# Performance work log

Measured on AMD Instinct MI355X. Metric: run time of the kernel, lower is better.

## Reference

```python
import jax, jax.numpy as jnp
import numpy as np

N = 100_000      # points
DEG = 16         # uniform neighbor count
E = N * DEG      # edges
NB = 4           # radial basis count (n)
MB = 4           # angular basis count (m)
FIN = 8
FOUT = 8
SUPPORT = 2.0    # module-level `support` constant in the original source


def _rbf_linear(nb, x, periodic):
    # evalRBFSeries(..., which='linear', epsilon=1.0): hat functions on [-1,1]
    if periodic:
        spacing = 2.0 / nb
        centroids = jnp.linspace(-1.0, 1.0, nb + 1)[:nb]          # [nb]
        ra = x[None, :] - centroids[:, None]                       # [nb, E]
        d = jnp.minimum(jnp.minimum(jnp.abs(ra), jnp.abs(ra - 2.0)), jnp.abs(ra + 2.0)) / spacing
    else:
        spacing = 2.0 / (nb - 1)
        centroids = jnp.linspace(-1.0, 1.0, nb)
        d = jnp.abs(x[None, :] - centroids[:, None]) / spacing     # [nb, E]
    return jnp.clip(1.0 - d, 0.0, 1.0)


def setup_inputs() -> dict:
    key = jax.random.key(0)
    k1, k2, k3, k4 = jax.random.split(key, 4)
    positions = jax.random.uniform(k1, (N, 2), dtype=jnp.float32)
    features = jax.random.normal(k2, (N, FIN), dtype=jnp.float32)
    # neighbors: DEG per point, never self (avoids zero-distance edges)
    offs = jax.random.randint(k3, (E,), 1, N)
    base = jnp.repeat(jnp.arange(N, dtype=jnp.int32), DEG)
    neighbors = ((base + offs) % N).astype(jnp.int32)
    row_splits = (jnp.arange(N + 1, dtype=jnp.int32) * DEG)
    # glorot_normal for kernel [fout, fin, n, m]
    kernel = jax.random.normal(k4, (FOUT, FIN, NB, MB), dtype=jnp.float32) * np.float32(
        np.sqrt(2.0 / ((FIN + FOUT) * NB * MB)))
    return {"positions": positions, "features": features, "kernel": kernel,
            "neighbors": neighbors, "row_splits": row_splits}


def reference(positions, features, kernel, neighbors, row_splits):
    n_pts = positions.shape[0]
    n_edges = neighbors.shape[0]
    counts = row_splits[1:] - row_splits[:-1]                       # [N]
    seg = jnp.repeat(jnp.arange(n_pts, dtype=jnp.int32), counts,
                     total_repeat_length=n_edges)                   # [E] owning point per edge
    rel = positions[neighbors] - positions[seg]                     # [E, 2]
    r = jnp.linalg.norm(rel, axis=1) / SUPPORT                      # [E]
    theta = jnp.arctan2(rel[:, 1], rel[:, 0])                       # [E]
    c = _rbf_linear(NB, r * 2.0 - 1.0, periodic=False)              # [NB, E]
    f = _rbf_linear(MB, theta / np.float32(np.pi), periodic=True)   # [MB, E]
    M = jnp.einsum('un,vn->nuv', c, f)                              # [E, NB, MB] per-edge outer product
    O = jnp.einsum('unm,ijnm->uij', M, kernel)                      # [E, FOUT, FIN]
    fv = features[neighbors]                                        # [E, FIN]
    FO = jnp.einsum('nij,nj->ni', O, fv)                            # [E, FOUT]
    return jax.ops.segment_sum(FO, seg, num_segments=n_pts)         # [N, FOUT]
```

## Files before the change

kernel.cpp:

```cpp
#include <hip/hip_runtime.h>
#include <math.h>


#define FIN 8
#define FOUT 8

__global__ __launch_bounds__(256) void rbf_kernel(
    const float* __restrict__ positions,
    const float* __restrict__ features,
    const float* __restrict__ kern,
    const int*   __restrict__ neighbors,
    const int*   __restrict__ row_splits,
    float*       __restrict__ out,
    int npts)
{
    __shared__ float Kl[1024];
    {
        const float4* src = (const float4*)kern;
        float4* dst = (float4*)Kl;
        if (threadIdx.x < 256) dst[threadIdx.x] = src[threadIdx.x];
    }
    __syncthreads();

    int gt   = blockIdx.x * blockDim.x + threadIdx.x;
    int u    = gt >> 1;
    int half = gt & 1;
    if (u >= npts) return;

    float2 pu = ((const float2*)positions)[u];
    int rs0 = row_splits[u];
    int rs1 = row_splits[u + 1];

    float g[16][4];
#pragma unroll
    for (int nm = 0; nm < 16; ++nm)
#pragma unroll
        for (int j = 0; j < 4; ++j) g[nm][j] = 0.0f;

    const float INV_PI = 0.31830988618379067f;

    for (int e = rs0; e < rs1; ++e) {
        int nb = neighbors[e];
        float2 pn = ((const float2*)positions)[nb];
        float dx = pn.x - pu.x;
        float dy = pn.y - pu.y;
        float dist = sqrtf(dx * dx + dy * dy);
        float tr = dist * 1.5f;
        float theta = atan2f(dy, dx);
        float ta = fmaf(theta, INV_PI, 1.0f) * 2.0f;

        float c[4], f[4];
#pragma unroll
        for (int n = 0; n < 4; ++n) {
            float d = fabsf(tr - (float)n);
            c[n] = fmaxf(1.0f - d, 0.0f);
        }
#pragma unroll
        for (int m = 0; m < 4; ++m) {
            float d0 = fabsf(ta - (float)m);
            float d1 = fabsf(ta - (float)m - 4.0f);
            float d2 = fabsf(ta - (float)m + 4.0f);
            float d  = fminf(d0, fminf(d1, d2));
            f[m] = fmaxf(1.0f - d, 0.0f);
        }

        float4 fv = ((const float4*)features)[nb * 2 + half];
        float fvj[4] = {fv.x, fv.y, fv.z, fv.w};

#pragma unroll
        for (int n = 0; n < 4; ++n)
#pragma unroll
            for (int m = 0; m < 4; ++m) {
                float w = c[n] * f[m];
#pragma unroll
                for (int j = 0; j < 4; ++j)
                    g[n * 4 + m][j] = fmaf(w, fvj[j], g[n * 4 + m][j]);
            }
    }

    float o[8];
#pragma unroll
    for (int i = 0; i < 8; ++i) o[i] = 0.0f;

    const float4* K4 = (const float4*)Kl;
#pragma unroll
    for (int i = 0; i < 8; ++i) {
#pragma unroll
        for (int j = 0; j < 4; ++j) {
            int jg = half * 4 + j;
            int base4 = (i * 128 + jg * 16) >> 2;
#pragma unroll
            for (int q = 0; q < 4; ++q) {
                float4 kv = K4[base4 + q];
                o[i] = fmaf(kv.x, g[q * 4 + 0][j], o[i]);
                o[i] = fmaf(kv.y, g[q * 4 + 1][j], o[i]);
                o[i] = fmaf(kv.z, g[q * 4 + 2][j], o[i]);
                o[i] = fmaf(kv.w, g[q * 4 + 3][j], o[i]);
            }
        }
    }

#pragma unroll
    for (int i = 0; i < 8; ++i)
        o[i] += __shfl_xor(o[i], 1);

    float4 ov = (half == 0) ? make_float4(o[0], o[1], o[2], o[3])
                            : make_float4(o[4], o[5], o[6], o[7]);
    ((float4*)out)[u * 2 + half] = ov;
}

extern "C" void kernel_launch(void* const* d_in, const int* in_sizes, int n_in,
                              void* d_out, int out_size, void* d_ws, size_t ws_size,
                              hipStream_t stream) {
    const float* positions  = (const float*)d_in[0];
    const float* features   = (const float*)d_in[1];
    const float* kern       = (const float*)d_in[2];
    const int*   neighbors  = (const int*)d_in[3];
    const int*   row_splits = (const int*)d_in[4];
    float* out = (float*)d_out;

    int npts = in_sizes[0] / 2;
    int total = npts * 2;
    int block = 256;
    int grid = (total + block - 1) / block;
    rbf_kernel<<<grid, block, 0, stream>>>(positions, features, kern,
                                           neighbors, row_splits, out, npts);
}
```

Before: 106.7 us.

## Split each point's edges across four lanes and batch neighbor gathers

Each point is now handled by four threads instead of two: two feature halves times two edge halves. Partial sums are combined with an extra xor-shuffle before the write. For the common 16-neighbor case, neighbor indices are read as int4 vectors and the position and feature gathers are issued four at a time, so more loads are in flight per thread. This doubles thread count and adds more latency hiding, at the cost of duplicated geometry and atan2 work across the feature halves and an extra shuffle stage.

```diff
diff --git a/kernel.cpp b/kernel.cpp
--- a/kernel.cpp
+++ b/kernel.cpp
@@ -23,13 +23,16 @@
     __syncthreads();
 
     int gt   = blockIdx.x * blockDim.x + threadIdx.x;
-    int u    = gt >> 1;
-    int half = gt & 1;
+    int u    = gt >> 2;
+    int sub  = gt & 3;
+    int half = sub & 1;
+    int eh   = sub >> 1;
     if (u >= npts) return;
 
     float2 pu = ((const float2*)positions)[u];
     int rs0 = row_splits[u];
     int rs1 = row_splits[u + 1];
+    int cnt = rs1 - rs0;
 
     float g[16][4];
 #pragma unroll
@@ -39,43 +42,101 @@
 
     const float INV_PI = 0.31830988618379067f;
 
-    for (int e = rs0; e < rs1; ++e) {
-        int nb = neighbors[e];
-        float2 pn = ((const float2*)positions)[nb];
-        float dx = pn.x - pu.x;
-        float dy = pn.y - pu.y;
-        float dist = sqrtf(dx * dx + dy * dy);
-        float tr = dist * 1.5f;
-        float theta = atan2f(dy, dx);
-        float ta = fmaf(theta, INV_PI, 1.0f) * 2.0f;
-
-        float c[4], f[4];
-#pragma unroll
-        for (int n = 0; n < 4; ++n) {
-            float d = fabsf(tr - (float)n);
-            c[n] = fmaxf(1.0f - d, 0.0f);
-        }
-#pragma unroll
-        for (int m = 0; m < 4; ++m) {
-            float d0 = fabsf(ta - (float)m);
-            float d1 = fabsf(ta - (float)m - 4.0f);
-            float d2 = fabsf(ta - (float)m + 4.0f);
-            float d  = fminf(d0, fminf(d1, d2));
-            f[m] = fmaxf(1.0f - d, 0.0f);
-        }
-
-        float4 fv = ((const float4*)features)[nb * 2 + half];
-        float fvj[4] = {fv.x, fv.y, fv.z, fv.w};
+    if (cnt == 16) {
+        int e0 = rs0 + eh * 8;
+        const int4* nb4 = (const int4*)(neighbors + e0);
+        int4 nbA = nb4[0];
+        int4 nbB = nb4[1];
 
 #pragma unroll
-        for (int n = 0; n < 4; ++n)
+        for (int grp = 0; grp < 2; ++grp) {
+            int nb[4];
+            {
+                int4 nv = (grp == 0) ? nbA : nbB;
+                nb[0] = nv.x; nb[1] = nv.y; nb[2] = nv.z; nb[3] = nv.w;
+            }
+            float2 pn[4];
+            float4 fv[4];
+#pragma unroll
+            for (int k = 0; k < 4; ++k) pn[k] = ((const float2*)positions)[nb[k]];
+#pragma unroll
+            for (int k = 0; k < 4; ++k) fv[k] = ((const float4*)features)[nb[k] * 2 + half];
+
+#pragma unroll
+            for (int k = 0; k < 4; ++k) {
+                float dx = pn[k].x - pu.x;
+                float dy = pn[k].y - pu.y;
+                float dist = sqrtf(dx * dx + dy * dy);
+                float tr = dist * 1.5f;
+                float theta = atan2f(dy, dx);
+                float ta = fmaf(theta, INV_PI, 1.0f) * 2.0f;
+
+                float c[4], f[4];
+#pragma unroll
+                for (int n = 0; n < 4; ++n) {
+                    float d = fabsf(tr - (float)n);
+                    c[n] = fmaxf(1.0f - d, 0.0f);
+                }
+#pragma unroll
+                for (int m = 0; m < 4; ++m) {
+                    float d0 = fabsf(ta - (float)m);
+                    float d1 = fabsf(ta - (float)m - 4.0f);
+                    float d2 = fabsf(ta - (float)m + 4.0f);
+                    float d  = fminf(d0, fminf(d1, d2));
+                    f[m] = fmaxf(1.0f - d, 0.0f);
+                }
+
+                float fvj[4] = {fv[k].x, fv[k].y, fv[k].z, fv[k].w};
+#pragma unroll
+                for (int n = 0; n < 4; ++n)
+#pragma unroll
+                    for (int m = 0; m < 4; ++m) {
+                        float w = c[n] * f[m];
+#pragma unroll
+                        for (int j = 0; j < 4; ++j)
+                            g[n * 4 + m][j] = fmaf(w, fvj[j], g[n * 4 + m][j]);
+                    }
+            }
+        }
+    } else {
+        int c0 = (cnt + 1) >> 1;
+        int e0 = rs0 + eh * c0;
+        int e1 = (eh == 0) ? (rs0 + c0) : rs1;
+        for (int e = e0; e < e1; ++e) {
+            int nb = neighbors[e];
+            float2 pn = ((const float2*)positions)[nb];
+            float dx = pn.x - pu.x;
+            float dy = pn.y - pu.y;
+            float dist = sqrtf(dx * dx + dy * dy);
+            float tr = dist * 1.5f;
+            float theta = atan2f(dy, dx);
+            float ta = fmaf(theta, INV_PI, 1.0f) * 2.0f;
+            float c[4], f[4];
+#pragma unroll
+            for (int n = 0; n < 4; ++n) {
+                float d = fabsf(tr - (float)n);
+                c[n] = fmaxf(1.0f - d, 0.0f);
+            }
 #pragma unroll
             for (int m = 0; m < 4; ++m) {
-                float w = c[n] * f[m];
+                float d0 = fabsf(ta - (float)m);
+                float d1 = fabsf(ta - (float)m - 4.0f);
+                float d2 = fabsf(ta - (float)m + 4.0f);
+                float d  = fminf(d0, fminf(d1, d2));
+                f[m] = fmaxf(1.0f - d, 0.0f);
+            }
+            float4 fv = ((const float4*)features)[nb * 2 + half];
+            float fvj[4] = {fv.x, fv.y, fv.z, fv.w};
 #pragma unroll
-                for (int j = 0; j < 4; ++j)
-                    g[n * 4 + m][j] = fmaf(w, fvj[j], g[n * 4 + m][j]);
-            }
+            for (int n = 0; n < 4; ++n)
+#pragma unroll
+                for (int m = 0; m < 4; ++m) {
+                    float w = c[n] * f[m];
+#pragma unroll
+                    for (int j = 0; j < 4; ++j)
+                        g[n * 4 + m][j] = fmaf(w, fvj[j], g[n * 4 + m][j]);
+                }
+        }
     }
 
     float o[8];
@@ -101,12 +162,16 @@
     }
 
 #pragma unroll
-    for (int i = 0; i < 8; ++i)
+    for (int i = 0; i < 8; ++i) {
         o[i] += __shfl_xor(o[i], 1);
+        o[i] += __shfl_xor(o[i], 2);
+    }
 
-    float4 ov = (half == 0) ? make_float4(o[0], o[1], o[2], o[3])
-                            : make_float4(o[4], o[5], o[6], o[7]);
-    ((float4*)out)[u * 2 + half] = ov;
+    float2 ov = (sub == 0) ? make_float2(o[0], o[1])
+              : (sub == 1) ? make_float2(o[2], o[3])
+              : (sub == 2) ? make_float2(o[4], o[5])
+                           : make_float2(o[6], o[7]);
+    ((float2*)out)[u * 4 + sub] = ov;
 }
 
 extern "C" void kernel_launch(void* const* d_in, const int* in_sizes, int n_in,
@@ -120,7 +185,7 @@
     float* out = (float*)d_out;
 
     int npts = in_sizes[0] / 2;
-    int total = npts * 2;
+    int total = npts * 4;
     int block = 256;
     int grid = (total + block - 1) / block;
     rbf_kernel<<<grid, block, 0, stream>>>(positions, features, kern,
```

Result: faster. 104.6 us (-2.0%).

## Use four threads per point, split edges, share basis via shuffles, fast atan2

Applied to the files above, without the earlier changes.

Each point is now handled by four threads instead of two: lanes split the edge list in halves and the feature channels in halves. In the 16-neighbor fast path each lane computes the radial and angular basis for only one edge of a pair and gets its partner's basis through lane shuffles, and all neighbor loads are issued up front from vectorized index reads. atan2 is replaced with a polynomial approximation, the periodic distance is simplified, and partial sums are reduced with an extra shuffle before a float2 store. This raises thread-level parallelism and removes duplicated transcendental work, at the cost of more threads, extra shuffles, and slight accuracy loss from the approximate atan2.

```diff
diff --git a/kernel.cpp b/kernel.cpp
--- a/kernel.cpp
+++ b/kernel.cpp
@@ -2,8 +2,43 @@
 #include <math.h>
 
 
-#define FIN 8
-#define FOUT 8
+#define TWO_OVER_PI 0.63661977236758134f
+
+__device__ __forceinline__ float fast_atan2f(float y, float x) {
+    float ax = fabsf(x), ay = fabsf(y);
+    float mx = fmaxf(ax, ay);
+    float mn = fminf(ax, ay);
+    mx = fmaxf(mx, 1e-30f);
+    float r = mn * __builtin_amdgcn_rcpf(mx);
+    float s = r * r;
+    float p = -0.0117212f;
+    p = fmaf(p, s,  0.05265332f);
+    p = fmaf(p, s, -0.11643287f);
+    p = fmaf(p, s,  0.19354346f);
+    p = fmaf(p, s, -0.33262347f);
+    p = fmaf(p, s,  0.99997726f);
+    float a = p * r;
+    a = (ay > ax) ? (1.57079632679f - a) : a;
+    a = (x < 0.0f) ? (3.14159265359f - a) : a;
+    return copysignf(a, y);
+}
+
+__device__ __forceinline__ void edge_basis(float dx, float dy,
+                                           float c[4], float f[4]) {
+    float dist = sqrtf(fmaf(dx, dx, dy * dy));
+    float tr = dist * 1.5f;
+    float theta = fast_atan2f(dy, dx);
+    float ta = fmaf(theta, TWO_OVER_PI, 2.0f);
+#pragma unroll
+    for (int n = 0; n < 4; ++n)
+        c[n] = fmaxf(1.0f - fabsf(tr - (float)n), 0.0f);
+#pragma unroll
+    for (int m = 0; m < 4; ++m) {
+        float d = fabsf(ta - (float)m);
+        d = fminf(d, 4.0f - d);
+        f[m] = fmaxf(1.0f - d, 0.0f);
+    }
+}
 
 __global__ __launch_bounds__(256) void rbf_kernel(
     const float* __restrict__ positions,
@@ -18,18 +53,21 @@
     {
         const float4* src = (const float4*)kern;
         float4* dst = (float4*)Kl;
-        if (threadIdx.x < 256) dst[threadIdx.x] = src[threadIdx.x];
+        dst[threadIdx.x] = src[threadIdx.x];
     }
     __syncthreads();
 
     int gt   = blockIdx.x * blockDim.x + threadIdx.x;
-    int u    = gt >> 1;
-    int half = gt & 1;
+    int u    = gt >> 2;
+    int sub  = gt & 3;
+    int half = sub & 1;
+    int eh   = sub >> 1;
     if (u >= npts) return;
 
     float2 pu = ((const float2*)positions)[u];
     int rs0 = row_splits[u];
     int rs1 = row_splits[u + 1];
+    int cnt = rs1 - rs0;
 
     float g[16][4];
 #pragma unroll
@@ -37,45 +75,84 @@
 #pragma unroll
         for (int j = 0; j < 4; ++j) g[nm][j] = 0.0f;
 
-    const float INV_PI = 0.31830988618379067f;
-
-    for (int e = rs0; e < rs1; ++e) {
-        int nb = neighbors[e];
-        float2 pn = ((const float2*)positions)[nb];
-        float dx = pn.x - pu.x;
-        float dy = pn.y - pu.y;
-        float dist = sqrtf(dx * dx + dy * dy);
-        float tr = dist * 1.5f;
-        float theta = atan2f(dy, dx);
-        float ta = fmaf(theta, INV_PI, 1.0f) * 2.0f;
-
-        float c[4], f[4];
-#pragma unroll
-        for (int n = 0; n < 4; ++n) {
-            float d = fabsf(tr - (float)n);
-            c[n] = fmaxf(1.0f - d, 0.0f);
+    const float2* pos2  = (const float2*)positions;
+    const float4* feat4 = (const float4*)features;
+
+    if (cnt == 16) {
+        int e0 = rs0 + eh * 8;
+        const int4* nb4 = (const int4*)(neighbors + e0);
+        int4 nA = nb4[0];
+        int4 nB = nb4[1];
+
+        int nbO0 = half ? nA.y : nA.x,  nbP0 = half ? nA.x : nA.y;
+        int nbO1 = half ? nA.w : nA.z,  nbP1 = half ? nA.z : nA.w;
+        int nbO2 = half ? nB.y : nB.x,  nbP2 = half ? nB.x : nB.y;
+        int nbO3 = half ? nB.w : nB.z,  nbP3 = half ? nB.z : nB.w;
+
+        float2 pO0 = pos2[nbO0];
+        float2 pO1 = pos2[nbO1];
+        float2 pO2 = pos2[nbO2];
+        float2 pO3 = pos2[nbO3];
+        float4 vO0 = feat4[nbO0 * 2 + half];
+        float4 vP0 = feat4[nbP0 * 2 + half];
+        float4 vO1 = feat4[nbO1 * 2 + half];
+        float4 vP1 = feat4[nbP1 * 2 + half];
+        float4 vO2 = feat4[nbO2 * 2 + half];
+        float4 vP2 = feat4[nbP2 * 2 + half];
+        float4 vO3 = feat4[nbO3 * 2 + half];
+        float4 vP3 = feat4[nbP3 * 2 + half];
+
+#define DO_PAIR(pO, vO, vP)                                                   \
+        {                                                                     \
+            float cO[4], fO[4], cP[4], fP[4];                                 \
+            edge_basis(pO.x - pu.x, pO.y - pu.y, cO, fO);                     \
+            _Pragma("unroll")                                                 \
+            for (int k = 0; k < 4; ++k) {                                     \
+                cP[k] = __shfl_xor(cO[k], 1);                                 \
+                fP[k] = __shfl_xor(fO[k], 1);                                 \
+            }                                                                 \
+            float aO[4] = {vO.x, vO.y, vO.z, vO.w};                           \
+            float aP[4] = {vP.x, vP.y, vP.z, vP.w};                           \
+            _Pragma("unroll")                                                 \
+            for (int n = 0; n < 4; ++n)                                       \
+                _Pragma("unroll")                                             \
+                for (int m = 0; m < 4; ++m) {                                 \
+                    float wO = cO[n] * fO[m];                                 \
+                    float wP = cP[n] * fP[m];                                 \
+                    _Pragma("unroll")                                         \
+                    for (int j = 0; j < 4; ++j) {                             \
+                        g[n * 4 + m][j] = fmaf(wO, aO[j], g[n * 4 + m][j]);   \
+                        g[n * 4 + m][j] = fmaf(wP, aP[j], g[n * 4 + m][j]);   \
+                    }                                                         \
+                }                                                             \
         }
-#pragma unroll
-        for (int m = 0; m < 4; ++m) {
-            float d0 = fabsf(ta - (float)m);
-            float d1 = fabsf(ta - (float)m - 4.0f);
-            float d2 = fabsf(ta - (float)m + 4.0f);
-            float d  = fminf(d0, fminf(d1, d2));
-            f[m] = fmaxf(1.0f - d, 0.0f);
+
+        DO_PAIR(pO0, vO0, vP0)
+        DO_PAIR(pO1, vO1, vP1)
+        DO_PAIR(pO2, vO2, vP2)
+        DO_PAIR(pO3, vO3, vP3)
+#undef DO_PAIR
+    } else {
+        int c0 = (cnt + 1) >> 1;
+        int e0 = rs0 + eh * c0;
+        int e1 = (eh == 0) ? (rs0 + c0) : rs1;
+        for (int e = e0; e < e1; ++e) {
+            int nb = neighbors[e];
+            float2 pn = pos2[nb];
+            float c[4], f[4];
+            edge_basis(pn.x - pu.x, pn.y - pu.y, c, f);
+            float4 fv = feat4[nb * 2 + half];
+            float fvj[4] = {fv.x, fv.y, fv.z, fv.w};
+#pragma unroll
+            for (int n = 0; n < 4; ++n)
+#pragma unroll
+                for (int m = 0; m < 4; ++m) {
+                    float w = c[n] * f[m];
+#pragma unroll
+                    for (int j = 0; j < 4; ++j)
+                        g[n * 4 + m][j] = fmaf(w, fvj[j], g[n * 4 + m][j]);
+                }
         }
-
-        float4 fv = ((const float4*)features)[nb * 2 + half];
-        float fvj[4] = {fv.x, fv.y, fv.z, fv.w};
-
-#pragma unroll
-        for (int n = 0; n < 4; ++n)
-#pragma unroll
-            for (int m = 0; m < 4; ++m) {
-                float w = c[n] * f[m];
-#pragma unroll
-                for (int j = 0; j < 4; ++j)
-                    g[n * 4 + m][j] = fmaf(w, fvj[j], g[n * 4 + m][j]);
-            }
     }
 
     float o[8];
@@ -101,12 +178,16 @@
     }
 
 #pragma unroll
-    for (int i = 0; i < 8; ++i)
+    for (int i = 0; i < 8; ++i) {
         o[i] += __shfl_xor(o[i], 1);
-
-    float4 ov = (half == 0) ? make_float4(o[0], o[1], o[2], o[3])
-                            : make_float4(o[4], o[5], o[6], o[7]);
-    ((float4*)out)[u * 2 + half] = ov;
+        o[i] += __shfl_xor(o[i], 2);
+    }
+
+    float2 ov = (sub == 0) ? make_float2(o[0], o[1])
+              : (sub == 1) ? make_float2(o[2], o[3])
+              : (sub == 2) ? make_float2(o[4], o[5])
+                           : make_float2(o[6], o[7]);
+    ((float2*)out)[u * 4 + sub] = ov;
 }
 
 extern "C" void kernel_launch(void* const* d_in, const int* in_sizes, int n_in,
@@ -120,7 +201,7 @@
     float* out = (float*)d_out;
 
     int npts = in_sizes[0] / 2;
-    int total = npts * 2;
+    int total = npts * 4;
     int block = 256;
     int grid = (total + block - 1) / block;
     rbf_kernel<<<grid, block, 0, stream>>>(positions, features, kern,
```

Measured after the change: 105.3 us. About the same (-1.3%).
